# Kernel optimization log

Measured on AMD Instinct MI355X. Metric: run time of the kernel, lower is better.

The kernel has to match this reference:

```python
import jax, jax.numpy as jnp
import numpy as np

N_EXPERTS = 256
N_GROUP = 8
TOPK_GROUP = 4
TOP_K = 8
ROUTED_SCALING = 2.5
HIDDEN = 7168


def setup_inputs() -> dict:
    key = jax.random.key(0)
    k1, k2, k3 = jax.random.split(key, 3)
    hidden_states = jax.random.normal(k1, (4, 4096, HIDDEN), dtype=jnp.float32)
    # kaiming_uniform(a=sqrt(5)) on [E, H] -> bound = 1/sqrt(H)
    bound = 1.0 / np.sqrt(HIDDEN)
    weight = jax.random.uniform(k2, (N_EXPERTS, HIDDEN), dtype=jnp.float32,
                                minval=-bound, maxval=bound)
    # buffer inits to zeros in torch; use small random values to exercise the bias path
    e_score_correction_bias = 0.01 * jax.random.normal(k3, (N_EXPERTS,), dtype=jnp.float32)
    return {"hidden_states": hidden_states, "weight": weight,
            "e_score_correction_bias": e_score_correction_bias}


def reference(hidden_states, weight, e_score_correction_bias):
    B, S, H = hidden_states.shape
    T = B * S
    x = hidden_states.reshape(T, H).astype(jnp.float32)
    # router logits: [T, E]
    logits = jnp.einsum('th,eh->te', x, weight)
    scores = jax.nn.sigmoid(logits)
    scores_for_choice = scores + e_score_correction_bias[None, :]
    # group score = sum of top-2 bias-adjusted scores within each group
    grp = scores_for_choice.reshape(T, N_GROUP, N_EXPERTS // N_GROUP)
    top2, _ = jax.lax.top_k(grp, 2)                      # [T, G, 2]
    group_scores = top2.sum(axis=-1)                     # [T, G]
    _, group_idx = jax.lax.top_k(group_scores, TOPK_GROUP)  # [T, topk_group]
    group_mask = jnp.zeros((T, N_GROUP), dtype=jnp.bool_)
    group_mask = group_mask.at[jnp.arange(T)[:, None], group_idx].set(True)
    score_mask = jnp.repeat(group_mask, N_EXPERTS // N_GROUP, axis=1)  # [T, E]
    masked_scores = jnp.where(score_mask, scores_for_choice, 0.0)
    _, topk_indices = jax.lax.top_k(masked_scores, TOP_K)  # [T, top_k]
    topk_weights = jnp.take_along_axis(scores, topk_indices, axis=1)
    denom = topk_weights.sum(axis=-1, keepdims=True) + 1e-20
    topk_weights = topk_weights / denom * ROUTED_SCALING
    return topk_indices, topk_weights
```

## Files before the change

### kernel.cpp

```cpp
#include <hip/hip_runtime.h>
#include <math.h>


#define HH 7168
#define EE 256
#define BMT 32
#define BK 32
#define NTH 128
#define TW 16
#define NT (HH / BK)

typedef float v4f __attribute__((ext_vector_type(4)));

struct SMem {
    union {
        float wbuf[2][EE * BK];
        float logits[BMT][EE];
    } u;
    float xbuf[2][BMT * BK];
    float bias[EE];
};

__device__ __forceinline__ void gl16(const void* g, void* l) {
    __builtin_amdgcn_global_load_lds(
        (__attribute__((address_space(1))) const void*)g,
        (__attribute__((address_space(3))) void*)l, 16, 0, 0);
}

#define LOADW(dst, wl, q) do { const int wq_ = (((q) ^ l7) << 2);            \
    dst[0] = *(const v4f*)&(wl)[(lane      ) * BK + wq_];                    \
    dst[1] = *(const v4f*)&(wl)[(lane +  64) * BK + wq_];                    \
    dst[2] = *(const v4f*)&(wl)[(lane + 128) * BK + wq_];                    \
    dst[3] = *(const v4f*)&(wl)[(lane + 192) * BK + wq_]; } while (0)

#define LOADX(dst, xl, q) do { _Pragma("unroll")                             \
    for (int t_ = 0; t_ < TW; ++t_)                                          \
        dst[t_] = *(const v4f*)&(xl)[t_ * BK + (q) * 4]; } while (0)

#define FMAB(xr, wr) do { _Pragma("unroll")                                  \
    for (int t_ = 0; t_ < TW; ++t_) { _Pragma("unroll")                      \
        for (int c_ = 0; c_ < 4; ++c_) {                                     \
            const float xs_ = xr[t_][c_];                                    \
            acc[t_][0] = fmaf(xs_, wr[0][c_], acc[t_][0]);                   \
            acc[t_][1] = fmaf(xs_, wr[1][c_], acc[t_][1]);                   \
            acc[t_][2] = fmaf(xs_, wr[2][c_], acc[t_][2]);                   \
            acc[t_][3] = fmaf(xs_, wr[3][c_], acc[t_][3]); } } } while (0)

__global__ __launch_bounds__(NTH, 1)
void moe_gate(const float* __restrict__ x, const float* __restrict__ w,
              const float* __restrict__ bias, float* __restrict__ out, int T) {
    __shared__ SMem sm;
    const int tid = threadIdx.x;
    const int bm = blockIdx.x * BMT;
    sm.bias[tid] = bias[tid];
    sm.bias[tid + 128] = bias[tid + 128];
    const int lane = tid & 63;
    const int wv = __builtin_amdgcn_readfirstlane(tid >> 6);
    const int l3 = (lane >> 3) & 7, l7 = lane & 7;

    const float* wsrc = w + (size_t)(wv * 128 + l3) * HH + ((l7 ^ l3) << 2);
    float* const wdst0 = &sm.u.wbuf[0][wv * 128 * BK];
    float* const wdst1 = &sm.u.wbuf[1][wv * 128 * BK];

    const int tok0 = tid >> 3;
    const float* xsrc0 = x + (size_t)(bm + tok0) * HH + (l7 << 2);
    const float* xsrc1 = xsrc0 + (size_t)16 * HH;
    float* const xd00 = &sm.xbuf[0][wv * 256];
    float* const xd01 = &sm.xbuf[0][wv * 256 + 512];
    float* const xd10 = &sm.xbuf[1][wv * 256];
    float* const xd11 = &sm.xbuf[1][wv * 256 + 512];

    float acc[TW][4];
    #pragma unroll
    for (int t = 0; t < TW; ++t)
        #pragma unroll
        for (int j = 0; j < 4; ++j) acc[t][j] = 0.f;

    #pragma unroll
    for (int p = 0; p < 16; ++p)
        gl16(wsrc + (size_t)p * 8 * HH, wdst0 + p * 8 * BK);
    gl16(xsrc0, xd00);
    gl16(xsrc1, xd01);
    __syncthreads();

    for (int ts = 0; ts < NT; ++ts) {
        const int b = ts & 1;
        if (ts + 1 < NT) {
            const int k1 = (ts + 1) * BK;
            float* wd = b ? wdst0 : wdst1;
            #pragma unroll
            for (int p = 0; p < 16; ++p)
                gl16(wsrc + (size_t)p * 8 * HH + k1, wd + p * 8 * BK);
            gl16(xsrc0 + k1, b ? xd00 : xd10);
            gl16(xsrc1 + k1, b ? xd01 : xd11);
        }
        const float* wl = b ? sm.u.wbuf[1] : sm.u.wbuf[0];
        const float* xl = (b ? &sm.xbuf[1][0] : &sm.xbuf[0][0]) + wv * 512;

        v4f wA[4], wB[4], xA[TW], xB[TW];
        LOADW(wA, wl, 0); LOADX(xA, xl, 0);
        LOADW(wB, wl, 1); LOADX(xB, xl, 1); FMAB(xA, wA);
        LOADW(wA, wl, 2); LOADX(xA, xl, 2); FMAB(xB, wB);
        LOADW(wB, wl, 3); LOADX(xB, xl, 3); FMAB(xA, wA);
        LOADW(wA, wl, 4); LOADX(xA, xl, 4); FMAB(xB, wB);
        LOADW(wB, wl, 5); LOADX(xB, xl, 5); FMAB(xA, wA);
        LOADW(wA, wl, 6); LOADX(xA, xl, 6); FMAB(xB, wB);
        LOADW(wB, wl, 7); LOADX(xB, xl, 7); FMAB(xA, wA);
        FMAB(xB, wB);
        __syncthreads();
    }

    #pragma unroll
    for (int t = 0; t < TW; ++t)
        #pragma unroll
        for (int j = 0; j < 4; ++j)
            sm.u.logits[wv * TW + t][lane + 64 * j] = acc[t][j];
    __syncthreads();

    for (int tt = wv; tt < BMT; tt += 2) {
        const int gt = bm + tt;
        float4 lg = *(const float4*)&sm.u.logits[tt][lane * 4];
        float lgv[4] = {lg.x, lg.y, lg.z, lg.w};
        float s[4], sc[4], m[4];
        #pragma unroll
        for (int j = 0; j < 4; ++j) {
            float e = (float)exp(-(double)lgv[j]);
            float u = __fadd_rn(1.0f, e);
            s[j] = __fdiv_rn(1.0f, u);
            sc[j] = __fadd_rn(s[j], sm.bias[lane * 4 + j]);
        }
        float a1 = fmaxf(sc[0], sc[1]), a2 = fminf(sc[0], sc[1]);
        if (sc[2] > a1) { a2 = a1; a1 = sc[2]; } else a2 = fmaxf(a2, sc[2]);
        if (sc[3] > a1) { a2 = a1; a1 = sc[3]; } else a2 = fmaxf(a2, sc[3]);
        #pragma unroll
        for (int off = 1; off <= 4; off <<= 1) {
            float b1 = __shfl_xor(a1, off);
            float b2 = __shfl_xor(a2, off);
            float m1 = fmaxf(a1, b1);
            float m2 = fmaxf(fminf(a1, b1), (a1 >= b1) ? a2 : b2);
            a1 = m1; a2 = m2;
        }
        float gsc = __fadd_rn(a1, a2);
        float gsv[8];
        #pragma unroll
        for (int g = 0; g < 8; ++g) gsv[g] = __shfl(gsc, g * 8);
        int gm = lane >> 3;
        int rank = 0;
        #pragma unroll
        for (int hh = 0; hh < 8; ++hh)
            rank += (gsv[hh] > gsv[gm]) || (gsv[hh] == gsv[gm] && hh > gm);
        bool selg = rank < 4;
        #pragma unroll
        for (int j = 0; j < 4; ++j) m[j] = selg ? sc[j] : 0.0f;

        float selw = 0.f; int seli = 0;
        #pragma unroll
        for (int k = 0; k < 8; ++k) {
            float bv = m[0]; int bj = 0;
            #pragma unroll
            for (int j = 1; j < 4; ++j)
                if (m[j] >= bv) { bv = m[j]; bj = j; }
            float v = bv; int ii = lane * 4 + bj;
            #pragma unroll
            for (int off = 1; off < 64; off <<= 1) {
                float ov = __shfl_xor(v, off);
                int oi = __shfl_xor(ii, off);
                if (ov > v || (ov == v && oi > ii)) { v = ov; ii = oi; }
            }
            int oj = ii & 3, ol = ii >> 2;
            float cand = (oj == 0) ? s[0] : (oj == 1) ? s[1]
                       : (oj == 2) ? s[2] : s[3];
            float wgt = __shfl(cand, ol);
            if (lane == k) { seli = ii; selw = wgt; }
            if (lane == ol) {
                if (oj == 0) m[0] = -1e30f;
                else if (oj == 1) m[1] = -1e30f;
                else if (oj == 2) m[2] = -1e30f;
                else m[3] = -1e30f;
            }
        }
        float wk[8];
        #pragma unroll
        for (int k = 0; k < 8; ++k) wk[k] = __shfl(selw, k);
        float denom = __fadd_rn(
            __fadd_rn(__fadd_rn(wk[0], wk[1]), __fadd_rn(wk[2], wk[3])),
            __fadd_rn(__fadd_rn(wk[4], wk[5]), __fadd_rn(wk[6], wk[7])));
        denom = __fadd_rn(denom, 1e-20f);
        if (lane < 8) {
            out[(size_t)gt * 8 + lane] = (float)seli;
            out[(size_t)T * 8 + (size_t)gt * 8 + lane] =
                __fmul_rn(__fdiv_rn(selw, denom), 2.5f);
        }
    }
}

extern "C" void kernel_launch(void* const* d_in, const int* in_sizes, int n_in,
                              void* d_out, int out_size, void* d_ws, size_t ws_size,
                              hipStream_t stream) {
    const float* x    = (const float*)d_in[0];
    const float* w    = (const float*)d_in[1];
    const float* bias = (const float*)d_in[2];
    float* out = (float*)d_out;
    const int T = in_sizes[0] / HH;
    moe_gate<<<T / BMT, NTH, 0, stream>>>(x, w, bias, out, T);
}
```

Baseline: 1.073 ms.

## Double block tile to 64 tokens with 256 threads and 8x8 register micro-tiles

Doubles the token tile per block from 32 to 64 and the thread count from 128 to 256 (4 waves). Each thread now computes an 8-token by 8-expert register tile instead of 16x4, with half-waves split across token sub-groups. The weight slice in LDS is shared by twice as many tokens, which halves the global weight traffic per token, and the more square micro-tile improves the FMA-to-LDS-load ratio. The cost is that the grid is halved to T/64 blocks, which may leave compute units underfilled, and the wider load pattern may change LDS bank behaviour.

```diff
diff --git a/kernel.cpp b/kernel.cpp
--- a/kernel.cpp
+++ b/kernel.cpp
@@ -4,10 +4,9 @@
 
 #define HH 7168
 #define EE 256
-#define BMT 32
+#define BMT 64
 #define BK 32
-#define NTH 128
-#define TW 16
+#define NTH 256
 #define NT (HH / BK)
 
 typedef float v4f __attribute__((ext_vector_type(4)));
@@ -27,24 +26,28 @@
         (__attribute__((address_space(3))) void*)l, 16, 0, 0);
 }
 
-#define LOADW(dst, wl, q) do { const int wq_ = (((q) ^ l7) << 2);            \
-    dst[0] = *(const v4f*)&(wl)[(lane      ) * BK + wq_];                    \
-    dst[1] = *(const v4f*)&(wl)[(lane +  64) * BK + wq_];                    \
-    dst[2] = *(const v4f*)&(wl)[(lane + 128) * BK + wq_];                    \
-    dst[3] = *(const v4f*)&(wl)[(lane + 192) * BK + wq_]; } while (0)
+#define LOADW(dst, wl, q) do {                                               \
+    const float* wp_ = (wl) + e5 * BK + (((q) ^ e3) << 2);                   \
+    dst[0] = *(const v4f*)(wp_ +   0 * BK);                                  \
+    dst[1] = *(const v4f*)(wp_ +  32 * BK);                                  \
+    dst[2] = *(const v4f*)(wp_ +  64 * BK);                                  \
+    dst[3] = *(const v4f*)(wp_ +  96 * BK);                                  \
+    dst[4] = *(const v4f*)(wp_ + 128 * BK);                                  \
+    dst[5] = *(const v4f*)(wp_ + 160 * BK);                                  \
+    dst[6] = *(const v4f*)(wp_ + 192 * BK);                                  \
+    dst[7] = *(const v4f*)(wp_ + 224 * BK); } while (0)
 
 #define LOADX(dst, xl, q) do { _Pragma("unroll")                             \
-    for (int t_ = 0; t_ < TW; ++t_)                                          \
-        dst[t_] = *(const v4f*)&(xl)[t_ * BK + (q) * 4]; } while (0)
+    for (int t_ = 0; t_ < 8; ++t_)                                           \
+        dst[t_] = *(const v4f*)((xl) + t_ * BK + (q) * 4); } while (0)
 
 #define FMAB(xr, wr) do { _Pragma("unroll")                                  \
-    for (int t_ = 0; t_ < TW; ++t_) { _Pragma("unroll")                      \
+    for (int t_ = 0; t_ < 8; ++t_) { _Pragma("unroll")                       \
         for (int c_ = 0; c_ < 4; ++c_) {                                     \
-            const float xs_ = xr[t_][c_];                                    \
-            acc[t_][0] = fmaf(xs_, wr[0][c_], acc[t_][0]);                   \
-            acc[t_][1] = fmaf(xs_, wr[1][c_], acc[t_][1]);                   \
-            acc[t_][2] = fmaf(xs_, wr[2][c_], acc[t_][2]);                   \
-            acc[t_][3] = fmaf(xs_, wr[3][c_], acc[t_][3]); } } } while (0)
+            const float xs_ = xr[t_][c_]; _Pragma("unroll")                  \
+            for (int j_ = 0; j_ < 8; ++j_)                                   \
+                acc[t_][j_] = fmaf(xs_, wr[j_][c_], acc[t_][j_]);            \
+        } } } while (0)
 
 __global__ __launch_bounds__(NTH, 1)
 void moe_gate(const float* __restrict__ x, const float* __restrict__ w,
@@ -53,34 +56,32 @@
     const int tid = threadIdx.x;
     const int bm = blockIdx.x * BMT;
     sm.bias[tid] = bias[tid];
-    sm.bias[tid + 128] = bias[tid + 128];
     const int lane = tid & 63;
     const int wv = __builtin_amdgcn_readfirstlane(tid >> 6);
+    const int p = lane >> 5;
+    const int e5 = lane & 31;
+    const int e3 = e5 & 7;
     const int l3 = (lane >> 3) & 7, l7 = lane & 7;
 
-    const float* wsrc = w + (size_t)(wv * 128 + l3) * HH + ((l7 ^ l3) << 2);
-    float* const wdst0 = &sm.u.wbuf[0][wv * 128 * BK];
-    float* const wdst1 = &sm.u.wbuf[1][wv * 128 * BK];
-
-    const int tok0 = tid >> 3;
-    const float* xsrc0 = x + (size_t)(bm + tok0) * HH + (l7 << 2);
-    const float* xsrc1 = xsrc0 + (size_t)16 * HH;
-    float* const xd00 = &sm.xbuf[0][wv * 256];
-    float* const xd01 = &sm.xbuf[0][wv * 256 + 512];
-    float* const xd10 = &sm.xbuf[1][wv * 256];
-    float* const xd11 = &sm.xbuf[1][wv * 256 + 512];
-
-    float acc[TW][4];
-    #pragma unroll
-    for (int t = 0; t < TW; ++t)
-        #pragma unroll
-        for (int j = 0; j < 4; ++j) acc[t][j] = 0.f;
-
-    #pragma unroll
-    for (int p = 0; p < 16; ++p)
-        gl16(wsrc + (size_t)p * 8 * HH, wdst0 + p * 8 * BK);
-    gl16(xsrc0, xd00);
-    gl16(xsrc1, xd01);
+    const float* wsrc = w + (size_t)(wv * 64 + l3) * HH + ((l7 ^ l3) << 2);
+    float* const wdst0 = &sm.u.wbuf[0][wv * 64 * BK];
+    float* const wdst1 = &sm.u.wbuf[1][wv * 64 * BK];
+    const float* xsrc = x + (size_t)(bm + wv * 16 + l3) * HH + (l7 << 2);
+    float* const xdst0 = &sm.xbuf[0][wv * 16 * BK];
+    float* const xdst1 = &sm.xbuf[1][wv * 16 * BK];
+
+    float acc[8][8];
+    #pragma unroll
+    for (int t = 0; t < 8; ++t)
+        #pragma unroll
+        for (int j = 0; j < 8; ++j) acc[t][j] = 0.f;
+
+    #pragma unroll
+    for (int p_ = 0; p_ < 8; ++p_)
+        gl16(wsrc + (size_t)p_ * 8 * HH, wdst0 + p_ * 8 * BK);
+    #pragma unroll
+    for (int i_ = 0; i_ < 2; ++i_)
+        gl16(xsrc + (size_t)i_ * 8 * HH, xdst0 + i_ * 8 * BK);
     __syncthreads();
 
     for (int ts = 0; ts < NT; ++ts) {
@@ -88,16 +89,18 @@
         if (ts + 1 < NT) {
             const int k1 = (ts + 1) * BK;
             float* wd = b ? wdst0 : wdst1;
-            #pragma unroll
-            for (int p = 0; p < 16; ++p)
-                gl16(wsrc + (size_t)p * 8 * HH + k1, wd + p * 8 * BK);
-            gl16(xsrc0 + k1, b ? xd00 : xd10);
-            gl16(xsrc1 + k1, b ? xd01 : xd11);
-        }
-        const float* wl = b ? sm.u.wbuf[1] : sm.u.wbuf[0];
-        const float* xl = (b ? &sm.xbuf[1][0] : &sm.xbuf[0][0]) + wv * 512;
-
-        v4f wA[4], wB[4], xA[TW], xB[TW];
+            float* xd = b ? xdst0 : xdst1;
+            #pragma unroll
+            for (int p_ = 0; p_ < 8; ++p_)
+                gl16(wsrc + (size_t)p_ * 8 * HH + k1, wd + p_ * 8 * BK);
+            #pragma unroll
+            for (int i_ = 0; i_ < 2; ++i_)
+                gl16(xsrc + (size_t)i_ * 8 * HH + k1, xd + i_ * 8 * BK);
+        }
+        const float* wl = sm.u.wbuf[b];
+        const float* xl = &sm.xbuf[b][(wv * 16 + p * 8) * BK];
+
+        v4f wA[8], wB[8], xA[8], xB[8];
         LOADW(wA, wl, 0); LOADX(xA, xl, 0);
         LOADW(wB, wl, 1); LOADX(xB, xl, 1); FMAB(xA, wA);
         LOADW(wA, wl, 2); LOADX(xA, xl, 2); FMAB(xB, wB);
@@ -111,13 +114,13 @@
     }
 
     #pragma unroll
-    for (int t = 0; t < TW; ++t)
-        #pragma unroll
-        for (int j = 0; j < 4; ++j)
-            sm.u.logits[wv * TW + t][lane + 64 * j] = acc[t][j];
+    for (int t = 0; t < 8; ++t)
+        #pragma unroll
+        for (int j = 0; j < 8; ++j)
+            sm.u.logits[wv * 16 + p * 8 + t][e5 + 32 * j] = acc[t][j];
     __syncthreads();
 
-    for (int tt = wv; tt < BMT; tt += 2) {
+    for (int tt = wv; tt < BMT; tt += 4) {
         const int gt = bm + tt;
         float4 lg = *(const float4*)&sm.u.logits[tt][lane * 4];
         float lgv[4] = {lg.x, lg.y, lg.z, lg.w};
```

Measured after the change: 1.119 ms. +4.2%, slower.
